# Kernel tuning notes

Hardware: AMD Instinct MI355X
Metric: run time of the kernel (lower is better)

The kernel has to match this reference:

```python
import jax, jax.numpy as jnp
import numpy as np

B, L, D, H = 4, 2048, 512, 8
HD = D // H
NEG = -1e9


def setup_inputs() -> dict:
    key = jax.random.key(0)
    ks = jax.random.split(key, 11)
    s = 1.0 / np.sqrt(D)
    inp = {
        "q": jax.random.normal(ks[0], (B, L, D), jnp.float32),
        "k": jax.random.normal(ks[1], (B, L, D), jnp.float32),
        "v": jax.random.normal(ks[2], (B, L, D), jnp.float32),
        "mask": jnp.broadcast_to(jnp.tril(jnp.ones((L, L), jnp.int32)), (B, L, L)),
        "Wq": jax.random.normal(ks[3], (D, D), jnp.float32) * s,
        "bq": jax.random.normal(ks[4], (D,), jnp.float32) * s,
        "Wk": jax.random.normal(ks[5], (D, D), jnp.float32) * s,
        "bk": jax.random.normal(ks[6], (D,), jnp.float32) * s,
        "Wv": jax.random.normal(ks[7], (D, D), jnp.float32) * s,
        "bv": jax.random.normal(ks[8], (D,), jnp.float32) * s,
        "Wo": jax.random.normal(ks[9], (D, D), jnp.float32) * s,
        "bo": jax.random.normal(ks[10], (D,), jnp.float32) * s,
    }
    return inp


def reference(q, k, v, mask, Wq, bq, Wk, bk, Wv, bv, Wo, bo):
    # Linear projections (torch Linear: x @ W.T + b)
    Q = (q @ Wq.T + bq).reshape(B, L, H, HD).transpose(0, 2, 1, 3)  # [B,H,L,hd]
    K = (k @ Wk.T + bk).reshape(B, L, H, HD).transpose(0, 2, 1, 3)
    V = (v @ Wv.T + bv).reshape(B, L, H, HD).transpose(0, 2, 1, 3)
    # scaled dot-product attention with masked_fill(mask==0, -1e9)
    score = jnp.einsum('bhqd,bhkd->bhqk', Q, K) / jnp.sqrt(jnp.float32(HD))
    score = jnp.where(mask[:, None, :, :] == 0, NEG, score)
    attn = jax.nn.softmax(score, axis=-1)
    ctx = jnp.einsum('bhqk,bhkd->bhqd', attn, V)  # [B,H,L,hd]
    ctx = ctx.transpose(0, 2, 1, 3).reshape(B, L, D)
    return ctx @ Wo.T + bo
```

## Files before the change

kernel.cpp:

```cpp
#include <hip/hip_runtime.h>
#include <hip/hip_bf16.h>
#include <math.h>

constexpr int Bc  = 4;
constexpr int Lc  = 2048;
constexpr int Dc  = 512;
constexpr int Hc  = 8;
constexpr int HDc = 64;

constexpr int GM = Bc * Lc;
constexpr int GK = Dc;
constexpr int BK = 64;

typedef __attribute__((ext_vector_type(8))) short bf16x8;
typedef __attribute__((ext_vector_type(4))) float f32x4;

static __device__ __forceinline__ short f2bf(float x) {
    __hip_bfloat16 h = __float2bfloat16(x);
    return (short)__builtin_bit_cast(unsigned short, h);
}

static __device__ __forceinline__ void gload_lds16(const void* g, void* l) {
    __builtin_amdgcn_global_load_lds(
        (const __attribute__((address_space(1))) void*)g,
        (__attribute__((address_space(3))) void*)l, 16, 0, 0);
}

__global__ __launch_bounds__(256)
void cast_all(const float* __restrict__ q, const float* __restrict__ k,
              const float* __restrict__ v, const float* __restrict__ wq,
              const float* __restrict__ wk, const float* __restrict__ wv,
              const float* __restrict__ wo, short* __restrict__ dst) {
    const size_t i = ((size_t)blockIdx.x * 256 + threadIdx.x) * 8;
    const float* src; size_t off;
    if      (i <  4194304) { src = q;  off = i; }
    else if (i <  8388608) { src = k;  off = i -  4194304; }
    else if (i < 12582912) { src = v;  off = i -  8388608; }
    else if (i < 12845056) { src = wq; off = i - 12582912; }
    else if (i < 13107200) { src = wk; off = i - 12845056; }
    else if (i < 13369344) { src = wv; off = i - 13107200; }
    else                   { src = wo; off = i - 13369344; }
    const float4 a = *(const float4*)(src + off);
    const float4 b = *(const float4*)(src + off + 4);
    bf16x8 o;
    o[0] = f2bf(a.x); o[1] = f2bf(a.y); o[2] = f2bf(a.z); o[3] = f2bf(a.w);
    o[4] = f2bf(b.x); o[5] = f2bf(b.y); o[6] = f2bf(b.z); o[7] = f2bf(b.w);
    *(bf16x8*)(dst + i) = o;
}

template<int BM, int BN, int WMT, int WNT>
__device__ __forceinline__ void gemm_tile(const short* __restrict__ A,
                                          const short* __restrict__ W,
                                          short* As, short* Bs,
                                          f32x4 (&acc)[WMT][WNT],
                                          int m0, int n0) {
    const int tid  = threadIdx.x;
    const int w    = tid >> 6;
    const int lane = tid & 63;
    const int low4 = lane & 15;
    const int quad = lane >> 4;
    const int wm   = w & 1, wn = w >> 1;
    const int lrow = lane >> 3;
    const int lchk = (lane & 7) * 8;

    for (int k0 = 0; k0 < GK; k0 += BK) {
#pragma unroll
        for (int i = 0; i < BM / 32; ++i) {
            const int r0 = i * 32 + w * 8;
            gload_lds16(A + (size_t)(m0 + r0 + lrow) * GK + k0 + lchk, As + r0 * BK);
        }
#pragma unroll
        for (int i = 0; i < BN / 32; ++i) {
            const int r0 = i * 32 + w * 8;
            gload_lds16(W + (size_t)(n0 + r0 + lrow) * GK + k0 + lchk, Bs + r0 * BK);
        }
        __syncthreads();
#pragma unroll
        for (int ks = 0; ks < 2; ++ks) {
            bf16x8 af[WMT], bfr[WNT];
#pragma unroll
            for (int mi = 0; mi < WMT; ++mi)
                af[mi] = *(const bf16x8*)(As + (wm * WMT * 16 + mi * 16 + low4) * BK + ks * 32 + quad * 8);
#pragma unroll
            for (int ni = 0; ni < WNT; ++ni)
                bfr[ni] = *(const bf16x8*)(Bs + (wn * WNT * 16 + ni * 16 + low4) * BK + ks * 32 + quad * 8);
#pragma unroll
            for (int mi = 0; mi < WMT; ++mi)
#pragma unroll
                for (int ni = 0; ni < WNT; ++ni)
                    acc[mi][ni] = __builtin_amdgcn_mfma_f32_16x16x32_bf16(af[mi], bfr[ni], acc[mi][ni], 0, 0, 0);
        }
        __syncthreads();
    }
}

__global__ __launch_bounds__(256)
void qkv_gemm(const short* __restrict__ Xq, const short* __restrict__ Xk,
              const short* __restrict__ Xv, const short* __restrict__ Wcat,
              const float* __restrict__ bq, const float* __restrict__ bk,
              const float* __restrict__ bv,
              short* __restrict__ Qw, short* __restrict__ Kw, short* __restrict__ Vw) {
    __shared__ __align__(16) short As[128 * BK];
    __shared__ __align__(16) short Bs[128 * BK];

    const int n0 = blockIdx.x * 128;
    const int m0 = blockIdx.y * 128;
    const int z  = n0 >> 9;
    const short* A    = (z == 0) ? Xq : (z == 1) ? Xk : Xv;
    const float* bias = (z == 0) ? bq : (z == 1) ? bk : bv;

    f32x4 acc[4][4];
#pragma unroll
    for (int mi = 0; mi < 4; ++mi)
#pragma unroll
        for (int ni = 0; ni < 4; ++ni) acc[mi][ni] = (f32x4){0.f, 0.f, 0.f, 0.f};

    gemm_tile<128, 128, 4, 4>(A, Wcat, As, Bs, acc, m0, n0);

    const int lane = threadIdx.x & 63, w = threadIdx.x >> 6;
    const int low4 = lane & 15, quad = lane >> 4;
    const int wm = w & 1, wn = w >> 1;
    short* Y = (z == 0) ? Qw : (z == 1) ? Kw : Vw;
#pragma unroll
    for (int mi = 0; mi < 4; ++mi)
#pragma unroll
        for (int ni = 0; ni < 4; ++ni)
#pragma unroll
            for (int r = 0; r < 4; ++r) {
                const int row = m0 + wm * 64 + mi * 16 + quad * 4 + r;
                const int col = n0 + wn * 64 + ni * 16 + low4;
                const int c   = col & 511;
                const float val = acc[mi][ni][r] + bias[c];
                const int b = row >> 11, l = row & 2047;
                const int h = c >> 6,    hd = c & 63;
                if (z < 2)
                    Y[(((size_t)b * Hc + h) * Lc + l) * HDc + hd] = f2bf(val);
                else
                    Y[(((size_t)b * Hc + h) * HDc + hd) * Lc + l] = f2bf(val);
            }
}

__global__ __launch_bounds__(256)
void out_gemm(const short* __restrict__ A, const short* __restrict__ W,
              const float* __restrict__ bias, float* __restrict__ Y) {
    __shared__ __align__(16) short As[64 * BK];
    __shared__ __align__(16) short Bs[128 * BK];

    const int n0 = blockIdx.x * 128;
    const int m0 = blockIdx.y * 64;

    f32x4 acc[2][4];
#pragma unroll
    for (int mi = 0; mi < 2; ++mi)
#pragma unroll
        for (int ni = 0; ni < 4; ++ni) acc[mi][ni] = (f32x4){0.f, 0.f, 0.f, 0.f};

    gemm_tile<64, 128, 2, 4>(A, W, As, Bs, acc, m0, n0);

    const int lane = threadIdx.x & 63, w = threadIdx.x >> 6;
    const int low4 = lane & 15, quad = lane >> 4;
    const int wm = w & 1, wn = w >> 1;
#pragma unroll
    for (int mi = 0; mi < 2; ++mi)
#pragma unroll
        for (int ni = 0; ni < 4; ++ni)
#pragma unroll
            for (int r = 0; r < 4; ++r) {
                const int row = m0 + wm * 32 + mi * 16 + quad * 4 + r;
                const int col = n0 + wn * 64 + ni * 16 + low4;
                Y[(size_t)row * Dc + col] = acc[mi][ni][r] + bias[col];
            }
}

__global__ __launch_bounds__(256)
void flash_attn(const short* __restrict__ Qb, const short* __restrict__ Kb,
                const short* __restrict__ VTb, short* __restrict__ ctx) {
    __shared__ __align__(16) short Kf[2][4096];
    __shared__ __align__(16) short Vf[2][4096];
    __shared__ __align__(16) short Ps[4][16 * 72];

    const int tid  = threadIdx.x;
    const int w    = tid >> 6;
    const int lane = tid & 63;
    const int low4 = lane & 15;
    const int quad = lane >> 4;

    const int bh = blockIdx.x & 31;
    const int qt = 31 - (blockIdx.x >> 5);
    const int q0  = qt * 64;
    const int q0w = q0 + w * 16;

    const short* Qg = Qb  + (size_t)bh * Lc * HDc;
    const short* Kg = Kb  + (size_t)bh * Lc * HDc;
    const short* Vg = VTb + (size_t)bh * HDc * Lc;

    const bf16x8 qa0 = *(const bf16x8*)(Qg + (size_t)(q0w + low4) * HDc + quad * 8);
    const bf16x8 qa1 = *(const bf16x8*)(Qg + (size_t)(q0w + low4) * HDc + 32 + quad * 8);

    f32x4 o[4];
    float lp[4] = {0.f, 0.f, 0.f, 0.f};
#pragma unroll
    for (int i = 0; i < 4; ++i) o[i] = (f32x4){0.f, 0.f, 0.f, 0.f};

#define STAGE(KT_, BUF_)                                                        \
    {                                                                           \
        _Pragma("unroll")                                                       \
        for (int p = 0; p < 2; ++p) {                                           \
            const int dc = w + 4 * p;                                           \
            gload_lds16(Kg + (size_t)((KT_) + lane) * HDc + dc * 8,             \
                        &Kf[BUF_][(dc * 64 + lane) * 8]);                       \
            gload_lds16(Vg + (size_t)lane * Lc + (KT_) + dc * 8,                \
                        &Vf[BUF_][(dc * 64 + lane) * 8]);                       \
        }                                                                       \
    }

    STAGE(0, 0);
    __syncthreads();

    for (int t = 0; t <= qt; ++t) {
        const int buf = t & 1;
        if (t < qt) STAGE((t + 1) * 64, buf ^ 1);

        f32x4 s[4];
#pragma unroll
        for (int nt = 0; nt < 4; ++nt) s[nt] = (f32x4){0.f, 0.f, 0.f, 0.f};
#pragma unroll
        for (int ks = 0; ks < 2; ++ks) {
            const bf16x8 qa = ks ? qa1 : qa0;
#pragma unroll
            for (int nt = 0; nt < 4; ++nt) {
                const bf16x8 kf = *(const bf16x8*)(&Kf[buf][((ks * 4 + quad) * 64 + nt * 16 + low4) * 8]);
                s[nt] = __builtin_amdgcn_mfma_f32_16x16x32_bf16(qa, kf, s[nt], 0, 0, 0);
            }
        }

        short* pw = Ps[w];
        const int kt = t * 64;
        if (t < qt) {
#pragma unroll
            for (int nt = 0; nt < 4; ++nt)
#pragma unroll
                for (int r = 0; r < 4; ++r) {
                    const float p = __expf(s[nt][r] * 0.125f);
                    lp[r] += p;
                    pw[(quad * 4 + r) * 72 + nt * 16 + low4] = f2bf(p);
                }
        } else {
#pragma unroll
            for (int nt = 0; nt < 4; ++nt)
#pragma unroll
                for (int r = 0; r < 4; ++r) {
                    const int qrow = q0w + quad * 4 + r;
                    const int col  = kt + nt * 16 + low4;
                    float p = __expf(s[nt][r] * 0.125f);
                    if (col > qrow) p = 0.f;
                    lp[r] += p;
                    pw[(quad * 4 + r) * 72 + nt * 16 + low4] = f2bf(p);
                }
        }

        __asm__ volatile("s_waitcnt lgkmcnt(0)" ::: "memory");

#pragma unroll
        for (int ks = 0; ks < 2; ++ks) {
            const bf16x8 pf = *(const bf16x8*)(pw + low4 * 72 + ks * 32 + quad * 8);
#pragma unroll
            for (int nt = 0; nt < 4; ++nt) {
                const bf16x8 vf = *(const bf16x8*)(&Vf[buf][((ks * 4 + quad) * 64 + nt * 16 + low4) * 8]);
                o[nt] = __builtin_amdgcn_mfma_f32_16x16x32_bf16(pf, vf, o[nt], 0, 0, 0);
            }
        }

        __syncthreads();
    }

#pragma unroll
    for (int off = 1; off < 16; off <<= 1)
#pragma unroll
        for (int r = 0; r < 4; ++r)
            lp[r] += __shfl_xor(lp[r], off, 64);

    const int b = bh >> 3, h = bh & 7;
#pragma unroll
    for (int r = 0; r < 4; ++r) {
        const float inv = 1.f / lp[r];
        const int q = q0w + quad * 4 + r;
#pragma unroll
        for (int nt = 0; nt < 4; ++nt)
            ctx[(size_t)(b * Lc + q) * Dc + h * HDc + nt * 16 + low4] = f2bf(o[nt][r] * inv);
    }
#undef STAGE
}

extern "C" void kernel_launch(void* const* d_in, const int* in_sizes, int n_in,
                              void* d_out, int out_size, void* d_ws, size_t ws_size,
                              hipStream_t stream) {
    const float* q  = (const float*)d_in[0];
    const float* k  = (const float*)d_in[1];
    const float* v  = (const float*)d_in[2];
    const float* Wq = (const float*)d_in[4];
    const float* bq = (const float*)d_in[5];
    const float* Wk = (const float*)d_in[6];
    const float* bk = (const float*)d_in[7];
    const float* Wv = (const float*)d_in[8];
    const float* bv = (const float*)d_in[9];
    const float* Wo = (const float*)d_in[10];
    const float* bo = (const float*)d_in[11];
    float* out = (float*)d_out;

    const size_t per = (size_t)Bc * Lc * Dc;
    const size_t wsz = (size_t)Dc * Dc;
    short* Xq  = (short*)d_ws;
    short* Xk  = Xq + per;
    short* Xv  = Xk + per;
    short* Wcat = Xv + per;
    short* Wob = Wcat + 3 * wsz;
    short* Qw  = Wob + wsz;
    short* Kw  = Qw + per;
    short* Vw  = Kw + per;
    short* Cw  = Vw + per;

    cast_all<<<6656, 256, 0, stream>>>(q, k, v, Wq, Wk, Wv, Wo, Xq);

    qkv_gemm<<<dim3(12, 64), 256, 0, stream>>>(Xq, Xk, Xv, Wcat,
                                               bq, bk, bv, Qw, Kw, Vw);

    flash_attn<<<Bc * Hc * (Lc / 64), 256, 0, stream>>>(Qw, Kw, Vw, Cw);

    out_gemm<<<dim3(4, 128), 256, 0, stream>>>(Cw, Wob, bo, out);
}
```

Baseline: 250.4 us.

## Pair causal query tiles per block and transpose V store through LDS

The flash attention kernel now gives each block two query tiles (pi and 31-pi) of the same head. Each block then does the same amount of causal work, and each staged K/V tile is reused for both query sets, with half as many blocks launched. The QKV GEMM epilogue for V now goes through a padded LDS tile, so the transposed V^T write becomes coalesced 16-byte stores instead of scattered 2-byte ones. The costs are higher register pressure from two sets of accumulators and a larger shared-memory buffer in the GEMM.

```diff
diff --git a/kernel.cpp b/kernel.cpp
--- a/kernel.cpp
+++ b/kernel.cpp
@@ -100,9 +100,12 @@
               const float* __restrict__ bq, const float* __restrict__ bk,
               const float* __restrict__ bv,
               short* __restrict__ Qw, short* __restrict__ Kw, short* __restrict__ Vw) {
-    __shared__ __align__(16) short As[128 * BK];
-    __shared__ __align__(16) short Bs[128 * BK];
-
+    __shared__ __align__(16) short Smem[128 * 136];
+    short* As = Smem;
+    short* Bs = Smem + 8192;
+    short* Ts = Smem;
+
+    const int tid = threadIdx.x;
     const int n0 = blockIdx.x * 128;
     const int m0 = blockIdx.y * 128;
     const int z  = n0 >> 9;
@@ -117,27 +120,49 @@
 
     gemm_tile<128, 128, 4, 4>(A, Wcat, As, Bs, acc, m0, n0);
 
-    const int lane = threadIdx.x & 63, w = threadIdx.x >> 6;
+    const int lane = tid & 63, w = tid >> 6;
     const int low4 = lane & 15, quad = lane >> 4;
     const int wm = w & 1, wn = w >> 1;
-    short* Y = (z == 0) ? Qw : (z == 1) ? Kw : Vw;
-#pragma unroll
-    for (int mi = 0; mi < 4; ++mi)
-#pragma unroll
-        for (int ni = 0; ni < 4; ++ni)
-#pragma unroll
-            for (int r = 0; r < 4; ++r) {
-                const int row = m0 + wm * 64 + mi * 16 + quad * 4 + r;
-                const int col = n0 + wn * 64 + ni * 16 + low4;
-                const int c   = col & 511;
-                const float val = acc[mi][ni][r] + bias[c];
-                const int b = row >> 11, l = row & 2047;
-                const int h = c >> 6,    hd = c & 63;
-                if (z < 2)
+
+    if (z < 2) {
+        short* Y = (z == 0) ? Qw : Kw;
+#pragma unroll
+        for (int mi = 0; mi < 4; ++mi)
+#pragma unroll
+            for (int ni = 0; ni < 4; ++ni)
+#pragma unroll
+                for (int r = 0; r < 4; ++r) {
+                    const int row = m0 + wm * 64 + mi * 16 + quad * 4 + r;
+                    const int col = n0 + wn * 64 + ni * 16 + low4;
+                    const int c   = col & 511;
+                    const float val = acc[mi][ni][r] + bias[c];
+                    const int b = row >> 11, l = row & 2047;
+                    const int h = c >> 6,    hd = c & 63;
                     Y[(((size_t)b * Hc + h) * Lc + l) * HDc + hd] = f2bf(val);
-                else
-                    Y[(((size_t)b * Hc + h) * HDc + hd) * Lc + l] = f2bf(val);
-            }
+                }
+    } else {
+#pragma unroll
+        for (int mi = 0; mi < 4; ++mi)
+#pragma unroll
+            for (int ni = 0; ni < 4; ++ni)
+#pragma unroll
+                for (int r = 0; r < 4; ++r) {
+                    const int rowL = wm * 64 + mi * 16 + quad * 4 + r;
+                    const int colL = wn * 64 + ni * 16 + low4;
+                    const int c    = (n0 + colL) & 511;
+                    Ts[colL * 136 + rowL] = f2bf(acc[mi][ni][r] + bias[c]);
+                }
+        __syncthreads();
+        const int hdl = tid >> 1, seg = tid & 1;
+        const int c  = (n0 + hdl) & 511;
+        const int h  = c >> 6, hd = c & 63;
+        const int b  = m0 >> 11, l0 = (m0 & 2047) + seg * 64;
+        short* dst = Vw + (((size_t)b * Hc + h) * HDc + hd) * Lc + l0;
+        const short* srcT = Ts + hdl * 136 + seg * 64;
+#pragma unroll
+        for (int j = 0; j < 8; ++j)
+            *(bf16x8*)(dst + j * 8) = *(const bf16x8*)(srcT + j * 8);
+    }
 }
 
 __global__ __launch_bounds__(256)
@@ -172,12 +197,40 @@
             }
 }
 
+__device__ __forceinline__ void softmax_rowset(const f32x4 (&s)[4], bool diag,
+                                               int qbase, int kt, short* pw,
+                                               float (&lp)[4],
+                                               int quad, int low4) {
+    if (!diag) {
+#pragma unroll
+        for (int nt = 0; nt < 4; ++nt)
+#pragma unroll
+            for (int r = 0; r < 4; ++r) {
+                const float p = __expf(s[nt][r] * 0.125f);
+                lp[r] += p;
+                pw[(quad * 4 + r) * 72 + nt * 16 + low4] = f2bf(p);
+            }
+    } else {
+#pragma unroll
+        for (int nt = 0; nt < 4; ++nt)
+#pragma unroll
+            for (int r = 0; r < 4; ++r) {
+                const int qrow = qbase + quad * 4 + r;
+                const int col  = kt + nt * 16 + low4;
+                float p = __expf(s[nt][r] * 0.125f);
+                if (col > qrow) p = 0.f;
+                lp[r] += p;
+                pw[(quad * 4 + r) * 72 + nt * 16 + low4] = f2bf(p);
+            }
+    }
+}
+
 __global__ __launch_bounds__(256)
 void flash_attn(const short* __restrict__ Qb, const short* __restrict__ Kb,
                 const short* __restrict__ VTb, short* __restrict__ ctx) {
     __shared__ __align__(16) short Kf[2][4096];
     __shared__ __align__(16) short Vf[2][4096];
-    __shared__ __align__(16) short Ps[4][16 * 72];
+    __shared__ __align__(16) short Ps[4][2][16*72];
 
     const int tid  = threadIdx.x;
     const int w    = tid >> 6;
@@ -185,22 +238,29 @@
     const int low4 = lane & 15;
     const int quad = lane >> 4;
 
-    const int bh = blockIdx.x & 31;
-    const int qt = 31 - (blockIdx.x >> 5);
-    const int q0  = qt * 64;
-    const int q0w = q0 + w * 16;
+    const int bh  = blockIdx.x & 31;
+    const int pi  = blockIdx.x >> 5;
+    const int qtA = pi;
+    const int qtB = 31 - pi;
+    const int qA0w = qtA * 64 + w * 16;
+    const int qB0w = qtB * 64 + w * 16;
 
     const short* Qg = Qb  + (size_t)bh * Lc * HDc;
     const short* Kg = Kb  + (size_t)bh * Lc * HDc;
     const short* Vg = VTb + (size_t)bh * HDc * Lc;
 
-    const bf16x8 qa0 = *(const bf16x8*)(Qg + (size_t)(q0w + low4) * HDc + quad * 8);
-    const bf16x8 qa1 = *(const bf16x8*)(Qg + (size_t)(q0w + low4) * HDc + 32 + quad * 8);
-
-    f32x4 o[4];
-    float lp[4] = {0.f, 0.f, 0.f, 0.f};
-#pragma unroll
-    for (int i = 0; i < 4; ++i) o[i] = (f32x4){0.f, 0.f, 0.f, 0.f};
+    const bf16x8 qaA0 = *(const bf16x8*)(Qg + (size_t)(qA0w + low4) * HDc + quad * 8);
+    const bf16x8 qaA1 = *(const bf16x8*)(Qg + (size_t)(qA0w + low4) * HDc + 32 + quad * 8);
+    const bf16x8 qaB0 = *(const bf16x8*)(Qg + (size_t)(qB0w + low4) * HDc + quad * 8);
+    const bf16x8 qaB1 = *(const bf16x8*)(Qg + (size_t)(qB0w + low4) * HDc + 32 + quad * 8);
+
+    f32x4 oA[4], oB[4];
+    float lpA[4] = {0.f, 0.f, 0.f, 0.f}, lpB[4] = {0.f, 0.f, 0.f, 0.f};
+#pragma unroll
+    for (int i = 0; i < 4; ++i) {
+        oA[i] = (f32x4){0.f, 0.f, 0.f, 0.f};
+        oB[i] = (f32x4){0.f, 0.f, 0.f, 0.f};
+    }
 
 #define STAGE(KT_, BUF_)                                                        \
     {                                                                           \
@@ -217,57 +277,63 @@
     STAGE(0, 0);
     __syncthreads();
 
-    for (int t = 0; t <= qt; ++t) {
+    for (int t = 0; t <= qtB; ++t) {
         const int buf = t & 1;
-        if (t < qt) STAGE((t + 1) * 64, buf ^ 1);
-
-        f32x4 s[4];
-#pragma unroll
-        for (int nt = 0; nt < 4; ++nt) s[nt] = (f32x4){0.f, 0.f, 0.f, 0.f};
+        if (t < qtB) STAGE((t + 1) * 64, buf ^ 1);
+        const int kt = t * 64;
+        const bool actA = (t <= qtA);
+
+        if (actA) {
+            f32x4 s[4];
+#pragma unroll
+            for (int nt = 0; nt < 4; ++nt) s[nt] = (f32x4){0.f, 0.f, 0.f, 0.f};
+#pragma unroll
+            for (int ks = 0; ks < 2; ++ks) {
+                const bf16x8 qa = ks ? qaA1 : qaA0;
+#pragma unroll
+                for (int nt = 0; nt < 4; ++nt) {
+                    const bf16x8 kf = *(const bf16x8*)(&Kf[buf][((ks * 4 + quad) * 64 + nt * 16 + low4) * 8]);
+                    s[nt] = __builtin_amdgcn_mfma_f32_16x16x32_bf16(qa, kf, s[nt], 0, 0, 0);
+                }
+            }
+            softmax_rowset(s, t == qtA, qA0w, kt, &Ps[w][0][0], lpA, quad, low4);
+        }
+        {
+            f32x4 s[4];
+#pragma unroll
+            for (int nt = 0; nt < 4; ++nt) s[nt] = (f32x4){0.f, 0.f, 0.f, 0.f};
+#pragma unroll
+            for (int ks = 0; ks < 2; ++ks) {
+                const bf16x8 qa = ks ? qaB1 : qaB0;
+#pragma unroll
+                for (int nt = 0; nt < 4; ++nt) {
+                    const bf16x8 kf = *(const bf16x8*)(&Kf[buf][((ks * 4 + quad) * 64 + nt * 16 + low4) * 8]);
+                    s[nt] = __builtin_amdgcn_mfma_f32_16x16x32_bf16(qa, kf, s[nt], 0, 0, 0);
+                }
+            }
+            softmax_rowset(s, t == qtB, qB0w, kt, &Ps[w][1][0], lpB, quad, low4);
+        }
+
+        __asm__ volatile("s_waitcnt lgkmcnt(0)" ::: "memory");
+
+        if (actA) {
+#pragma unroll
+            for (int ks = 0; ks < 2; ++ks) {
+                const bf16x8 pf = *(const bf16x8*)(&Ps[w][0][0] + low4 * 72 + ks * 32 + quad * 8);
+#pragma unroll
+                for (int nt = 0; nt < 4; ++nt) {
+                    const bf16x8 vf = *(const bf16x8*)(&Vf[buf][((ks * 4 + quad) * 64 + nt * 16 + low4) * 8]);
+                    oA[nt] = __builtin_amdgcn_mfma_f32_16x16x32_bf16(pf, vf, oA[nt], 0, 0, 0);
+                }
+            }
+        }
 #pragma unroll
         for (int ks = 0; ks < 2; ++ks) {
-            const bf16x8 qa = ks ? qa1 : qa0;
-#pragma unroll
-            for (int nt = 0; nt < 4; ++nt) {
-                const bf16x8 kf = *(const bf16x8*)(&Kf[buf][((ks * 4 + quad) * 64 + nt * 16 + low4) * 8]);
-                s[nt] = __builtin_amdgcn_mfma_f32_16x16x32_bf16(qa, kf, s[nt], 0, 0, 0);
-            }
-        }
-
-        short* pw = Ps[w];
-        const int kt = t * 64;
-        if (t < qt) {
-#pragma unroll
-            for (int nt = 0; nt < 4; ++nt)
-#pragma unroll
-                for (int r = 0; r < 4; ++r) {
-                    const float p = __expf(s[nt][r] * 0.125f);
-                    lp[r] += p;
-                    pw[(quad * 4 + r) * 72 + nt * 16 + low4] = f2bf(p);
-                }
-        } else {
-#pragma unroll
-            for (int nt = 0; nt < 4; ++nt)
-#pragma unroll
-                for (int r = 0; r < 4; ++r) {
-                    const int qrow = q0w + quad * 4 + r;
-                    const int col  = kt + nt * 16 + low4;
-                    float p = __expf(s[nt][r] * 0.125f);
-                    if (col > qrow) p = 0.f;
-                    lp[r] += p;
-                    pw[(quad * 4 + r) * 72 + nt * 16 + low4] = f2bf(p);
-                }
-        }
-
-        __asm__ volatile("s_waitcnt lgkmcnt(0)" ::: "memory");
-
-#pragma unroll
-        for (int ks = 0; ks < 2; ++ks) {
-            const bf16x8 pf = *(const bf16x8*)(pw + low4 * 72 + ks * 32 + quad * 8);
+            const bf16x8 pf = *(const bf16x8*)(&Ps[w][1][0] + low4 * 72 + ks * 32 + quad * 8);
 #pragma unroll
             for (int nt = 0; nt < 4; ++nt) {
                 const bf16x8 vf = *(const bf16x8*)(&Vf[buf][((ks * 4 + quad) * 64 + nt * 16 + low4) * 8]);
-                o[nt] = __builtin_amdgcn_mfma_f32_16x16x32_bf16(pf, vf, o[nt], 0, 0, 0);
+                oB[nt] = __builtin_amdgcn_mfma_f32_16x16x32_bf16(pf, vf, oB[nt], 0, 0, 0);
             }
         }
 
@@ -277,17 +343,23 @@
 #pragma unroll
     for (int off = 1; off < 16; off <<= 1)
 #pragma unroll
-        for (int r = 0; r < 4; ++r)
-            lp[r] += __shfl_xor(lp[r], off, 64);
+        for (int r = 0; r < 4; ++r) {
+            lpA[r] += __shfl_xor(lpA[r], off, 64);
+            lpB[r] += __shfl_xor(lpB[r], off, 64);
+        }
 
     const int b = bh >> 3, h = bh & 7;
 #pragma unroll
     for (int r = 0; r < 4; ++r) {
-        const float inv = 1.f / lp[r];
-        const int q = q0w + quad * 4 + r;
-#pragma unroll
-        for (int nt = 0; nt < 4; ++nt)
-            ctx[(size_t)(b * Lc + q) * Dc + h * HDc + nt * 16 + low4] = f2bf(o[nt][r] * inv);
+        const float invA = 1.f / lpA[r];
+        const float invB = 1.f / lpB[r];
+        const int qA = qA0w + quad * 4 + r;
+        const int qB = qB0w + quad * 4 + r;
+#pragma unroll
+        for (int nt = 0; nt < 4; ++nt) {
+            ctx[(size_t)(b * Lc + qA) * Dc + h * HDc + nt * 16 + low4] = f2bf(oA[nt][r] * invA);
+            ctx[(size_t)(b * Lc + qB) * Dc + h * HDc + nt * 16 + low4] = f2bf(oB[nt][r] * invB);
+        }
     }
 #undef STAGE
 }
@@ -325,7 +397,7 @@
     qkv_gemm<<<dim3(12, 64), 256, 0, stream>>>(Xq, Xk, Xv, Wcat,
                                                bq, bk, bv, Qw, Kw, Vw);
 
-    flash_attn<<<Bc * Hc * (Lc / 64), 256, 0, stream>>>(Qw, Kw, Vw, Cw);
+    flash_attn<<<512, 256, 0, stream>>>(Qw, Kw, Vw, Cw);
 
     out_gemm<<<dim3(4, 128), 256, 0, stream>>>(Cw, Wob, bo, out);
 }
```

New measurement: 240.2 us. 1.04x faster.
